# Kernel tuning notes

Hardware: AMD Instinct MI355X
Metric: run time of the kernel (lower is better)

## Reference

```python
import jax, jax.numpy as jnp
import numpy as np

N = 32768
D = 256
NUM_POS = 4
TEMPS = 2
ID_NUM = N // TEMPS // NUM_POS  # 4096


def setup_inputs() -> dict:
    key = jax.random.key(0)
    k1, _ = jax.random.split(key)
    inputs = jax.random.normal(k1, (N, D), dtype=jnp.float32)
    # two modality halves, each half = each id repeated NUM_POS times
    targets = (jnp.arange(N, dtype=jnp.int64) // NUM_POS) % ID_NUM
    return {"inputs": inputs, "targets": targets}


def reference(inputs, targets):
    eps = 1e-6
    num_pos, temps = NUM_POS, TEMPS
    n = inputs.shape[0]
    id_num = n // temps // num_pos

    # centers: per-id mean (original python loop over ids == segment mean)
    ones = jnp.ones((n,), inputs.dtype)
    counts = jax.ops.segment_sum(ones, targets, num_segments=id_num)  # [id_num]
    centers = jax.ops.segment_sum(inputs, targets, num_segments=id_num) / counts[:, None]  # [id_num, D]

    # pairwise euclidean distance centers -> inputs  [id_num, N]
    d2 = (jnp.sum(centers * centers, axis=1)[:, None]
          + jnp.sum(inputs * inputs, axis=1)[None, :]
          - 2.0 * centers @ inputs.T)
    dist = jnp.sqrt(jnp.clip(d2, 1e-12, None))

    # is_neg_c2i: id of each center vs every sample
    center_ids = targets[jnp.arange(id_num) * num_pos]  # [id_num]
    is_neg = center_ids[:, None] != targets[None, :]    # [id_num, N]

    # negative mining (masked, fixed-shape version of an[an>1e-6].view)
    an = jnp.where(is_neg, dist, 0.0)
    valid_neg = an > eps
    n_neg = jnp.sum(valid_neg, axis=1).astype(dist.dtype)           # = N - temps*num_pos
    d_neg = jnp.sum(jnp.where(valid_neg, an, 0.0), axis=1) / n_neg  # per-center mean neg dist
    hard = valid_neg & (an < d_neg[:, None])                        # hard negatives (closer than mean)
    hard_cnt = jnp.sum(hard, axis=1).astype(dist.dtype)
    row_an = jnp.sum(jnp.where(hard, an, 0.0), axis=1) / hard_cnt   # per-center hard-neg mean
    an_mean = jnp.mean(row_an)

    # positives: center to its own samples
    ap = jnp.where(is_neg, 0.0, dist)
    valid_pos = ap > eps
    ap_mean = jnp.sum(jnp.where(valid_pos, ap, 0.0)) / jnp.sum(valid_pos).astype(dist.dtype)

    return ap_mean / an_mean
```

## Files before the change

kernel.cpp:

```cpp
#include <hip/hip_runtime.h>
#include <hip/hip_bf16.h>

#define NS   32768
#define DD   256
#define NPOS 4
#define IDN  4096

#define QSCALE 15.9375f
#define QBIAS  (-158.875f)
#define QINV   0.0627451f

typedef __attribute__((ext_vector_type(8))) short short8;
typedef __attribute__((ext_vector_type(4))) float f32x4;

__device__ __forceinline__ unsigned short f2bf(float f) {
    unsigned int u = __builtin_bit_cast(unsigned int, f);
    unsigned int r = (u + 0x7FFFu + ((u >> 16) & 1u)) >> 16;
    return (unsigned short)r;
}

__device__ __forceinline__ void gload16(const void* g, void* lds) {
    __builtin_amdgcn_global_load_lds(
        (const __attribute__((address_space(1))) unsigned int*)g,
        (__attribute__((address_space(3))) unsigned int*)lds, 16, 0, 0);
}

__device__ __forceinline__ float qdequant(unsigned int q) {
    return fmaf((float)q, QINV, 10.0f);
}
__device__ __forceinline__ unsigned int qquant(float d) {
    float t = fmaf(d, QSCALE, QBIAS);
    t = fminf(255.0f, fmaxf(0.0f, t));
    return (unsigned int)t;
}


__global__ void conv_k(const float* __restrict__ in, unsigned short* __restrict__ Xb,
                       float* __restrict__ x2) {
    int row  = blockIdx.x * 4 + (threadIdx.x >> 6);
    int lane = threadIdx.x & 63;
    const float4 v = *(const float4*)&in[(size_t)row * DD + lane * 4];
    ushort4 u;
    u.x = f2bf(v.x); u.y = f2bf(v.y); u.z = f2bf(v.z); u.w = f2bf(v.w);
    *(ushort4*)&Xb[(size_t)row * DD + lane * 4] = u;
    float sq = v.x * v.x + v.y * v.y + v.z * v.z + v.w * v.w;
    #pragma unroll
    for (int m = 1; m < 64; m <<= 1) sq += __shfl_xor(sq, m, 64);
    if (lane == 0) x2[row] = sq;
}

__global__ void centers_k(const float* __restrict__ in,
                          unsigned short* __restrict__ Cb, float* __restrict__ c2) {
    int r = blockIdx.x, d = threadIdx.x;
    const float* p0 = in + (size_t)(4 * r) * DD + d;
    const float* p1 = in + (size_t)(16384 + 4 * r) * DD + d;
    float s = 0.f;
    #pragma unroll
    for (int j = 0; j < 4; ++j) s += p0[(size_t)j * DD];
    #pragma unroll
    for (int j = 0; j < 4; ++j) s += p1[(size_t)j * DD];
    float mean = s * 0.125f;
    Cb[(size_t)r * DD + d] = f2bf(mean);
    float sq = mean * mean;
    #pragma unroll
    for (int m = 1; m < 64; m <<= 1) sq += __shfl_xor(sq, m, 64);
    __shared__ float sb[4];
    int lane = d & 63, w = d >> 6;
    if (lane == 0) sb[w] = sq;
    __syncthreads();
    if (d == 0) c2[r] = sb[0] + sb[1] + sb[2] + sb[3];
}

__global__ __launch_bounds__(256)
void pos_k(const float* __restrict__ in, const float* __restrict__ c2,
           const float* __restrict__ x2,
           float* __restrict__ possum, float* __restrict__ posdist) {
    const int r = blockIdx.x * 4 + (threadIdx.x >> 6);
    const int l = threadIdx.x & 63;
    float cx = 0.f, cy = 0.f, cz = 0.f, cw = 0.f;
    #pragma unroll
    for (int j = 0; j < 8; ++j) {
        const int rr = (j < 4) ? (4 * r + j) : (16384 + 4 * r + (j - 4));
        const float4 v = *(const float4*)&in[(size_t)rr * DD + l * 4];
        cx += v.x; cy += v.y; cz += v.z; cw += v.w;
    }
    cx *= 0.125f; cy *= 0.125f; cz *= 0.125f; cw *= 0.125f;
    const float c2v = c2[r];
    float ps = 0.f;
    #pragma unroll
    for (int j = 0; j < 8; ++j) {
        const int cc = (j < 4) ? (4 * r + j) : (16384 + 4 * r + (j - 4));
        const float4 xv = *(const float4*)&in[(size_t)cc * DD + l * 4];
        float p = cx * xv.x + cy * xv.y + cz * xv.z + cw * xv.w;
        #pragma unroll
        for (int m = 1; m < 64; m <<= 1) p += __shfl_xor(p, m, 64);
        float d2 = c2v + x2[cc] - 2.f * p;
        float dist = sqrtf(fmaxf(d2, 1e-12f));
        ps += dist;
        if (l == 0) posdist[r * 8 + j] = dist;
    }
    if (l == 0) possum[r] = ps;
}

__global__ void dneg_k(const float* __restrict__ negsum_all,
                       const float* __restrict__ possum,
                       const float* __restrict__ posdist,
                       float* __restrict__ dnout,
                       float* __restrict__ pcs, float* __restrict__ pcc, int mode) {
    int r = blockIdx.x * 256 + threadIdx.x;
    if (r < IDN) {
        float dn = (negsum_all[r] - possum[r]) * (1.0f / 32760.0f);
        dnout[r] = mode ? dn : dn * dn;
        float s = 0.f, c = 0.f;
        #pragma unroll
        for (int j = 0; j < 8; ++j) {
            float d = posdist[r * 8 + j];
            if (mode) d = qdequant(qquant(d));
            if (d < dn) { s += d; c += 1.f; }
        }
        pcs[r] = s; pcc[r] = c;
    }
}


template <bool STORE>
__global__ __launch_bounds__(512, 2)
void mpass1_k(const unsigned short* __restrict__ Cb, const unsigned short* __restrict__ Xb,
              const float* __restrict__ c2, const float* __restrict__ x2,
              float* __restrict__ S, unsigned char* __restrict__ D2) {
    __shared__ unsigned short As[64 * 512];
    __shared__ unsigned short Bs[2 * 32 * 512];

    const int tid = threadIdx.x;
    const int l  = tid & 63;
    const int w  = tid >> 6;
    const int wr = w >> 2;
    const int wc = w & 3;
    const int lr = l & 15;
    const int lc = l >> 4;
    const int bid = blockIdx.x;
    const int ch = bid & 7;
    const int bm = bid >> 3;
    const int colbase = ch * 4096;

    const unsigned short* bj[4]; unsigned int bslot[4];
    #pragma unroll
    for (int j = 0; j < 4; ++j) {
        const int s = w * 4 + j;
        const int kk2s = s >> 4;
        const int cbs  = s & 15;
        bj[j] = Xb + (size_t)(colbase + cbs * 16 + lr) * DD + kk2s * 32 + lc * 8;
        bslot[j] = (unsigned)(kk2s * 16 + cbs) * 512;
    }

    {
        const unsigned short* asrc = Cb + (size_t)(bm * 128 + lr) * DD + w * 32 + lc * 8;
        #pragma unroll
        for (int rb = 0; rb < 8; ++rb)
            gload16(asrc + (size_t)rb * 16 * DD, &As[(w * 8 + rb) * 512]);
        #pragma unroll
        for (int j = 0; j < 4; ++j)
            gload16(bj[j], &Bs[bslot[j]]);
    }
    __syncthreads();

    const int gr0 = bm * 128 + wr * 64;
    float c2v[16];
    #pragma unroll
    for (int mf = 0; mf < 4; ++mf)
        #pragma unroll
        for (int r = 0; r < 4; ++r)
            c2v[mf * 4 + r] = c2[gr0 + mf * 16 + lc * 4 + r];

    float rs[16];
    #pragma unroll
    for (int i = 0; i < 16; ++i) rs[i] = 0.f;

    unsigned char* dbase = STORE ? (D2 + (size_t)bid * 524288 + (size_t)w * 1024 + l * 16)
                                 : nullptr;

    for (int step = 0; step < 16; ++step) {
        float x2v[4];
        #pragma unroll
        for (int nf = 0; nf < 4; ++nf)
            x2v[nf] = x2[colbase + step * 256 + wc * 64 + nf * 16 + lr];

        f32x4 acc[4][4];
        #pragma unroll
        for (int a = 0; a < 4; ++a)
            #pragma unroll
            for (int b = 0; b < 4; ++b) acc[a][b] = (f32x4){0.f, 0.f, 0.f, 0.f};

        #pragma unroll
        for (int ss = 0; ss < 4; ++ss) {
            const int g  = step * 4 + ss;
            const int gn = (g + 1) & 63;
            {
                const size_t go = (size_t)(gn >> 2) * (256 * DD) + (gn & 3) * 64;
                const unsigned int doff = (unsigned)(gn & 1) * 16384;
                #pragma unroll
                for (int j = 0; j < 4; ++j)
                    gload16(bj[j] + go, &Bs[doff + bslot[j]]);
            }
            const unsigned int boff = (unsigned)(g & 1) * 16384;
            #pragma unroll
            for (int kk2 = 0; kk2 < 2; ++kk2) {
                const int kkg = ss * 2 + kk2;
                short8 af[4], bf[4];
                #pragma unroll
                for (int mf = 0; mf < 4; ++mf)
                    af[mf] = *(const short8*)&As[((kkg * 8) + wr * 4 + mf) * 512 + l * 8];
                #pragma unroll
                for (int nf = 0; nf < 4; ++nf)
                    bf[nf] = *(const short8*)&Bs[boff + (kk2 * 16 + wc * 4 + nf) * 512 + l * 8];
                __builtin_amdgcn_s_setprio(1);
                #pragma unroll
                for (int mf = 0; mf < 4; ++mf)
                    #pragma unroll
                    for (int nf = 0; nf < 4; ++nf)
                        acc[mf][nf] = __builtin_amdgcn_mfma_f32_16x16x32_bf16(
                            af[mf], bf[nf], acc[mf][nf], 0, 0, 0);
                __builtin_amdgcn_s_setprio(0);
            }
            __syncthreads();
        }

        #pragma unroll
        for (int mf = 0; mf < 4; ++mf) {
            unsigned int pw[4];
            #pragma unroll
            for (int r = 0; r < 4; ++r) {
                const int i = mf * 4 + r;
                unsigned int b = 0;
                #pragma unroll
                for (int nf = 0; nf < 4; ++nf) {
                    float d2 = fmaf(-2.f, acc[mf][nf][r], c2v[i] + x2v[nf]);
                    float dist = __builtin_amdgcn_sqrtf(fmaxf(d2, 1e-12f));
                    rs[i] += dist;
                    if (STORE) b |= qquant(dist) << (8 * nf);
                }
                pw[r] = b;
            }
            if (STORE) {
                uint4 v; v.x = pw[0]; v.y = pw[1]; v.z = pw[2]; v.w = pw[3];
                *(uint4*)(dbase + (size_t)(step * 4 + mf) * 8192) = v;
            }
        }
    }

    #pragma unroll
    for (int i = 0; i < 16; ++i)
        #pragma unroll
        for (int m = 1; m < 16; m <<= 1)
            rs[i] += __shfl_xor(rs[i], m, 64);
    if (lr == 0) {
        #pragma unroll
        for (int mf = 0; mf < 4; ++mf)
            #pragma unroll
            for (int r = 0; r < 4; ++r)
                atomicAdd(&S[gr0 + mf * 16 + lc * 4 + r], rs[mf * 4 + r]);
    }
}

__global__ __launch_bounds__(512)
void hard_k(const unsigned char* __restrict__ D2, const float* __restrict__ dn,
            float* __restrict__ S, float* __restrict__ C) {
    const int tid = threadIdx.x;
    const int l  = tid & 63;
    const int w  = tid >> 6;
    const int wr = w >> 2;
    const int lc = l >> 4;
    const int lr = l & 15;
    const int bid2 = blockIdx.x;
    const int obid = bid2 >> 2;
    const int sub  = bid2 & 3;
    const int bm = obid >> 3;
    const int gr0 = bm * 128 + wr * 64;

    float dnv[16];
    #pragma unroll
    for (int mf = 0; mf < 4; ++mf)
        #pragma unroll
        for (int r = 0; r < 4; ++r)
            dnv[mf * 4 + r] = dn[gr0 + mf * 16 + lc * 4 + r];

    float rs[16], rc[16];
    #pragma unroll
    for (int i = 0; i < 16; ++i) { rs[i] = 0.f; rc[i] = 0.f; }

    const unsigned char* dbase = D2 + (size_t)obid * 524288 + (size_t)w * 1024 + l * 16;

    for (int s4 = 0; s4 < 4; ++s4) {
        const int step = sub * 4 + s4;
        #pragma unroll
        for (int mf = 0; mf < 4; ++mf) {
            uint4 v = *(const uint4*)(dbase + (size_t)(step * 4 + mf) * 8192);
            unsigned int pw[4] = {v.x, v.y, v.z, v.w};
            #pragma unroll
            for (int r = 0; r < 4; ++r) {
                const int i = mf * 4 + r;
                const float dni = dnv[i];
                #pragma unroll
                for (int nf = 0; nf < 4; ++nf) {
                    float d = qdequant((pw[r] >> (8 * nf)) & 0xFFu);
                    if (d < dni) { rs[i] += d; rc[i] += 1.f; }
                }
            }
        }
    }

    #pragma unroll
    for (int i = 0; i < 16; ++i)
        #pragma unroll
        for (int m = 1; m < 16; m <<= 1) {
            rs[i] += __shfl_xor(rs[i], m, 64);
            rc[i] += __shfl_xor(rc[i], m, 64);
        }
    if (lr == 0) {
        #pragma unroll
        for (int mf = 0; mf < 4; ++mf)
            #pragma unroll
            for (int r = 0; r < 4; ++r) {
                const int row = gr0 + mf * 16 + lc * 4 + r;
                atomicAdd(&S[row], rs[mf * 4 + r]);
                atomicAdd(&C[row], rc[mf * 4 + r]);
            }
    }
}

__global__ __launch_bounds__(512, 2)
void mpass2_k(const unsigned short* __restrict__ Cb, const unsigned short* __restrict__ Xb,
              const float* __restrict__ c2, const float* __restrict__ x2,
              const float* __restrict__ dneg2,
              float* __restrict__ S, float* __restrict__ C) {
    __shared__ unsigned short As[64 * 512];
    __shared__ unsigned short Bs[2 * 32 * 512];
    const int tid = threadIdx.x;
    const int l  = tid & 63;
    const int w  = tid >> 6;
    const int wr = w >> 2;
    const int wc = w & 3;
    const int lr = l & 15;
    const int lc = l >> 4;
    const int bid = blockIdx.x;
    const int ch = bid & 7;
    const int bm = bid >> 3;
    const int colbase = ch * 4096;
    const unsigned short* bj[4]; unsigned int bslot[4];
    #pragma unroll
    for (int j = 0; j < 4; ++j) {
        const int s = w * 4 + j;
        const int kk2s = s >> 4, cbs = s & 15;
        bj[j] = Xb + (size_t)(colbase + cbs * 16 + lr) * DD + kk2s * 32 + lc * 8;
        bslot[j] = (unsigned)(kk2s * 16 + cbs) * 512;
    }
    {
        const unsigned short* asrc = Cb + (size_t)(bm * 128 + lr) * DD + w * 32 + lc * 8;
        #pragma unroll
        for (int rb = 0; rb < 8; ++rb)
            gload16(asrc + (size_t)rb * 16 * DD, &As[(w * 8 + rb) * 512]);
        #pragma unroll
        for (int j = 0; j < 4; ++j) gload16(bj[j], &Bs[bslot[j]]);
    }
    __syncthreads();
    const int gr0 = bm * 128 + wr * 64;
    float c2v[16], dnv[16];
    #pragma unroll
    for (int mf = 0; mf < 4; ++mf)
        #pragma unroll
        for (int r = 0; r < 4; ++r) {
            const int row = gr0 + mf * 16 + lc * 4 + r;
            c2v[mf * 4 + r] = c2[row];
            dnv[mf * 4 + r] = dneg2[row];
        }
    float rs[16], rc[16];
    #pragma unroll
    for (int i = 0; i < 16; ++i) { rs[i] = 0.f; rc[i] = 0.f; }
    for (int step = 0; step < 16; ++step) {
        float x2v[4];
        #pragma unroll
        for (int nf = 0; nf < 4; ++nf)
            x2v[nf] = x2[colbase + step * 256 + wc * 64 + nf * 16 + lr];
        f32x4 acc[4][4];
        #pragma unroll
        for (int a = 0; a < 4; ++a)
            #pragma unroll
            for (int b = 0; b < 4; ++b) acc[a][b] = (f32x4){0.f, 0.f, 0.f, 0.f};
        #pragma unroll
        for (int ss = 0; ss < 4; ++ss) {
            const int g = step * 4 + ss, gn = (g + 1) & 63;
            {
                const size_t go = (size_t)(gn >> 2) * (256 * DD) + (gn & 3) * 64;
                const unsigned int doff = (unsigned)(gn & 1) * 16384;
                #pragma unroll
                for (int j = 0; j < 4; ++j) gload16(bj[j] + go, &Bs[doff + bslot[j]]);
            }
            const unsigned int boff = (unsigned)(g & 1) * 16384;
            #pragma unroll
            for (int kk2 = 0; kk2 < 2; ++kk2) {
                const int kkg = ss * 2 + kk2;
                short8 af[4], bf[4];
                #pragma unroll
                for (int mf = 0; mf < 4; ++mf)
                    af[mf] = *(const short8*)&As[((kkg * 8) + wr * 4 + mf) * 512 + l * 8];
                #pragma unroll
                for (int nf = 0; nf < 4; ++nf)
                    bf[nf] = *(const short8*)&Bs[boff + (kk2 * 16 + wc * 4 + nf) * 512 + l * 8];
                __builtin_amdgcn_s_setprio(1);
                #pragma unroll
                for (int mf = 0; mf < 4; ++mf)
                    #pragma unroll
                    for (int nf = 0; nf < 4; ++nf)
                        acc[mf][nf] = __builtin_amdgcn_mfma_f32_16x16x32_bf16(
                            af[mf], bf[nf], acc[mf][nf], 0, 0, 0);
                __builtin_amdgcn_s_setprio(0);
            }
            __syncthreads();
        }
        #pragma unroll
        for (int mf = 0; mf < 4; ++mf)
            #pragma unroll
            for (int nf = 0; nf < 4; ++nf)
                #pragma unroll
                for (int r = 0; r < 4; ++r) {
                    const int i = mf * 4 + r;
                    float d2 = fmaf(-2.f, acc[mf][nf][r], c2v[i] + x2v[nf]);
                    float d2c = fmaxf(d2, 1e-12f);
                    bool h = d2c < dnv[i];
                    rs[i] += h ? __builtin_amdgcn_sqrtf(d2c) : 0.f;
                    rc[i] += h ? 1.f : 0.f;
                }
    }
    #pragma unroll
    for (int i = 0; i < 16; ++i)
        #pragma unroll
        for (int m = 1; m < 16; m <<= 1) {
            rs[i] += __shfl_xor(rs[i], m, 64);
            rc[i] += __shfl_xor(rc[i], m, 64);
        }
    if (lr == 0) {
        #pragma unroll
        for (int mf = 0; mf < 4; ++mf)
            #pragma unroll
            for (int r = 0; r < 4; ++r) {
                const int row = gr0 + mf * 16 + lc * 4 + r;
                atomicAdd(&S[row], rs[mf * 4 + r]);
                atomicAdd(&C[row], rc[mf * 4 + r]);
            }
    }
}

__global__ void final_k(const float* __restrict__ hardsum,
                        const float* __restrict__ hardcnt,
                        const float* __restrict__ pcs, const float* __restrict__ pcc,
                        const float* __restrict__ possum, float* out) {
    float s_an = 0.f, s_ap = 0.f;
    for (int r = threadIdx.x; r < IDN; r += 256) {
        s_an += (hardsum[r] - pcs[r]) / fmaxf(hardcnt[r] - pcc[r], 1.0f);
        s_ap += possum[r];
    }
    #pragma unroll
    for (int m = 1; m < 64; m <<= 1) {
        s_an += __shfl_xor(s_an, m, 64);
        s_ap += __shfl_xor(s_ap, m, 64);
    }
    __shared__ float sb[8];
    int lane = threadIdx.x & 63, w = threadIdx.x >> 6;
    if (lane == 0) { sb[w] = s_an; sb[4 + w] = s_ap; }
    __syncthreads();
    if (threadIdx.x == 0) {
        float an = (sb[0] + sb[1] + sb[2] + sb[3]) / (float)IDN;
        float ap = (sb[4] + sb[5] + sb[6] + sb[7]) / (float)NS;
        out[0] = ap / an;
    }
}


extern "C" void kernel_launch(void* const* d_in, const int* in_sizes, int n_in,
                              void* d_out, int out_size, void* d_ws, size_t ws_size,
                              hipStream_t stream) {
    const float* inputs = (const float*)d_in[0];
    float* out = (float*)d_out;

    char* p = (char*)d_ws;
    unsigned short* Xb = (unsigned short*)p;  p += (size_t)NS * DD * 2;
    unsigned short* Cb = (unsigned short*)p;  p += (size_t)IDN * DD * 2;
    float* x2      = (float*)p;  p += (size_t)NS * 4;
    float* c2      = (float*)p;  p += (size_t)IDN * 4;
    float* dnbuf   = (float*)p;  p += (size_t)IDN * 4;
    float* possum  = (float*)p;  p += (size_t)IDN * 4;
    float* posdist = (float*)p;  p += (size_t)IDN * 8 * 4;
    float* pcs     = (float*)p;  p += (size_t)IDN * 4;
    float* pcc     = (float*)p;  p += (size_t)IDN * 4;
    char* zp = p;
    float* negsum  = (float*)p;  p += (size_t)IDN * 4;
    float* hardsum = (float*)p;  p += (size_t)IDN * 4;
    float* hardcnt = (float*)p;  p += (size_t)IDN * 4;
    p = (char*)(((size_t)p + 255) & ~(size_t)255);
    unsigned char* D2 = (unsigned char*)p;
    size_t required_big = (size_t)(p - (char*)d_ws) + (size_t)NS * IDN;

    const bool big = (ws_size >= required_big);

    hipMemsetAsync(zp, 0, (size_t)(3 * IDN * 4), stream);
    conv_k<<<NS / 4, 256, 0, stream>>>(inputs, Xb, x2);
    centers_k<<<IDN, 256, 0, stream>>>(inputs, Cb, c2);
    pos_k<<<IDN / 4, 256, 0, stream>>>(inputs, c2, x2, possum, posdist);

    if (big) {
        mpass1_k<true><<<256, 512, 0, stream>>>(Cb, Xb, c2, x2, negsum, D2);
        dneg_k<<<IDN / 256, 256, 0, stream>>>(negsum, possum, posdist, dnbuf, pcs, pcc, 1);
        hard_k<<<1024, 512, 0, stream>>>(D2, dnbuf, hardsum, hardcnt);
    } else {
        mpass1_k<false><<<256, 512, 0, stream>>>(Cb, Xb, c2, x2, negsum, nullptr);
        dneg_k<<<IDN / 256, 256, 0, stream>>>(negsum, possum, posdist, dnbuf, pcs, pcc, 0);
        mpass2_k<<<256, 512, 0, stream>>>(Cb, Xb, c2, x2, dnbuf, hardsum, hardcnt);
    }
    final_k<<<1, 256, 0, stream>>>(hardsum, hardcnt, pcs, pcc, possum, out);
}
```

Before: 240.0 us.

## Fuse conversion, center, and positive-distance prep kernels into one pass

```diff
diff --git a/kernel.cpp b/kernel.cpp
--- a/kernel.cpp
+++ b/kernel.cpp
@@ -35,71 +35,63 @@
 }
 
 
-__global__ void conv_k(const float* __restrict__ in, unsigned short* __restrict__ Xb,
-                       float* __restrict__ x2) {
-    int row  = blockIdx.x * 4 + (threadIdx.x >> 6);
-    int lane = threadIdx.x & 63;
-    const float4 v = *(const float4*)&in[(size_t)row * DD + lane * 4];
-    ushort4 u;
-    u.x = f2bf(v.x); u.y = f2bf(v.y); u.z = f2bf(v.z); u.w = f2bf(v.w);
-    *(ushort4*)&Xb[(size_t)row * DD + lane * 4] = u;
-    float sq = v.x * v.x + v.y * v.y + v.z * v.z + v.w * v.w;
-    #pragma unroll
-    for (int m = 1; m < 64; m <<= 1) sq += __shfl_xor(sq, m, 64);
-    if (lane == 0) x2[row] = sq;
-}
-
-__global__ void centers_k(const float* __restrict__ in,
-                          unsigned short* __restrict__ Cb, float* __restrict__ c2) {
-    int r = blockIdx.x, d = threadIdx.x;
-    const float* p0 = in + (size_t)(4 * r) * DD + d;
-    const float* p1 = in + (size_t)(16384 + 4 * r) * DD + d;
-    float s = 0.f;
-    #pragma unroll
-    for (int j = 0; j < 4; ++j) s += p0[(size_t)j * DD];
-    #pragma unroll
-    for (int j = 0; j < 4; ++j) s += p1[(size_t)j * DD];
-    float mean = s * 0.125f;
-    Cb[(size_t)r * DD + d] = f2bf(mean);
-    float sq = mean * mean;
-    #pragma unroll
-    for (int m = 1; m < 64; m <<= 1) sq += __shfl_xor(sq, m, 64);
-    __shared__ float sb[4];
-    int lane = d & 63, w = d >> 6;
-    if (lane == 0) sb[w] = sq;
+__global__ __launch_bounds__(256)
+void prep_k(const float* __restrict__ in, unsigned short* __restrict__ Xb,
+            float* __restrict__ x2, unsigned short* __restrict__ Cb,
+            float* __restrict__ c2, float* __restrict__ possum,
+            float* __restrict__ posdist) {
+    const int r = blockIdx.x;
+    const int d = threadIdx.x;
+    const int lane = d & 63, wv = d >> 6;
+
+    int rows[8];
+    #pragma unroll
+    for (int j = 0; j < 8; ++j)
+        rows[j] = (j < 4) ? (4 * r + j) : (16384 + 4 * r + (j - 4));
+
+    float v[8];
+    #pragma unroll
+    for (int j = 0; j < 8; ++j) v[j] = in[(size_t)rows[j] * DD + d];
+
+    float c = (v[0] + v[1] + v[2] + v[3] + v[4] + v[5] + v[6] + v[7]) * 0.125f;
+    Cb[(size_t)r * DD + d] = f2bf(c);
+    #pragma unroll
+    for (int j = 0; j < 8; ++j)
+        Xb[(size_t)rows[j] * DD + d] = f2bf(v[j]);
+
+    float part[17];
+    #pragma unroll
+    for (int j = 0; j < 8; ++j) { part[j] = v[j] * v[j]; part[8 + j] = c * v[j]; }
+    part[16] = c * c;
+    #pragma unroll
+    for (int k = 0; k < 17; ++k)
+        #pragma unroll
+        for (int m = 1; m < 64; m <<= 1)
+            part[k] += __shfl_xor(part[k], m, 64);
+
+    __shared__ float red2[17][4];
+    __shared__ float fin[17];
+    __shared__ float pdsh[8];
+    if (lane == 0)
+        #pragma unroll
+        for (int k = 0; k < 17; ++k) red2[k][wv] = part[k];
     __syncthreads();
-    if (d == 0) c2[r] = sb[0] + sb[1] + sb[2] + sb[3];
-}
-
-__global__ __launch_bounds__(256)
-void pos_k(const float* __restrict__ in, const float* __restrict__ c2,
-           const float* __restrict__ x2,
-           float* __restrict__ possum, float* __restrict__ posdist) {
-    const int r = blockIdx.x * 4 + (threadIdx.x >> 6);
-    const int l = threadIdx.x & 63;
-    float cx = 0.f, cy = 0.f, cz = 0.f, cw = 0.f;
-    #pragma unroll
-    for (int j = 0; j < 8; ++j) {
-        const int rr = (j < 4) ? (4 * r + j) : (16384 + 4 * r + (j - 4));
-        const float4 v = *(const float4*)&in[(size_t)rr * DD + l * 4];
-        cx += v.x; cy += v.y; cz += v.z; cw += v.w;
-    }
-    cx *= 0.125f; cy *= 0.125f; cz *= 0.125f; cw *= 0.125f;
-    const float c2v = c2[r];
-    float ps = 0.f;
-    #pragma unroll
-    for (int j = 0; j < 8; ++j) {
-        const int cc = (j < 4) ? (4 * r + j) : (16384 + 4 * r + (j - 4));
-        const float4 xv = *(const float4*)&in[(size_t)cc * DD + l * 4];
-        float p = cx * xv.x + cy * xv.y + cz * xv.z + cw * xv.w;
-        #pragma unroll
-        for (int m = 1; m < 64; m <<= 1) p += __shfl_xor(p, m, 64);
-        float d2 = c2v + x2[cc] - 2.f * p;
+    if (d < 17) fin[d] = red2[d][0] + red2[d][1] + red2[d][2] + red2[d][3];
+    __syncthreads();
+
+    if (d < 8) {
+        x2[rows[d]] = fin[d];
+        float d2 = fin[16] + fin[d] - 2.f * fin[8 + d];
         float dist = sqrtf(fmaxf(d2, 1e-12f));
-        ps += dist;
-        if (l == 0) posdist[r * 8 + j] = dist;
-    }
-    if (l == 0) possum[r] = ps;
+        posdist[r * 8 + d] = dist;
+        pdsh[d] = dist;
+    }
+    __syncthreads();
+    if (d == 0) {
+        c2[r] = fin[16];
+        possum[r] = pdsh[0] + pdsh[1] + pdsh[2] + pdsh[3]
+                  + pdsh[4] + pdsh[5] + pdsh[6] + pdsh[7];
+    }
 }
 
 __global__ void dneg_k(const float* __restrict__ negsum_all,
@@ -503,9 +495,7 @@
     const bool big = (ws_size >= required_big);
 
     hipMemsetAsync(zp, 0, (size_t)(3 * IDN * 4), stream);
-    conv_k<<<NS / 4, 256, 0, stream>>>(inputs, Xb, x2);
-    centers_k<<<IDN, 256, 0, stream>>>(inputs, Cb, c2);
-    pos_k<<<IDN / 4, 256, 0, stream>>>(inputs, c2, x2, possum, posdist);
+    prep_k<<<IDN, 256, 0, stream>>>(inputs, Xb, x2, Cb, c2, possum, posdist);
 
     if (big) {
         mpass1_k<true><<<256, 512, 0, stream>>>(Cb, Xb, c2, x2, negsum, D2);
```

Result: no change. 239.8 us (-0.1%).
